# Kernel optimization log

Measured on AMD Instinct MI355X. Metric: run time of the kernel, lower is better.

Reference implementation:

```python
import jax, jax.numpy as jnp
import numpy as np

B, N, H, HEADS = 4, 512, 256, 8
SUBH = H // HEADS
FF = 4 * H
EPS = 1e-5


def _layernorm(x, g, b):
    m = jnp.mean(x, axis=-1, keepdims=True)
    v = jnp.mean(jnp.square(x - m), axis=-1, keepdims=True)
    return (x - m) * jax.lax.rsqrt(v + EPS) * g + b


def setup_inputs() -> dict:
    key = jax.random.key(0)
    ks = jax.random.split(key, 10)
    sc = 0.02
    return {
        "S": jax.random.normal(ks[0], (B, N, H), dtype=jnp.float32),
        "T": jax.random.normal(ks[1], (B, N, N, H), dtype=jnp.float32),
        "masks": jnp.ones((B, N), dtype=bool),
        "Wqk": jax.random.normal(ks[2], (H, HEADS), dtype=jnp.float32) * sc,
        "Wv": jax.random.normal(ks[3], (H, H), dtype=jnp.float32) * sc,
        "bv": jnp.zeros((H,), dtype=jnp.float32),
        "Wo": jax.random.normal(ks[4], (H, H), dtype=jnp.float32) * sc,
        "bo": jnp.zeros((H,), dtype=jnp.float32),
        "g0": jnp.ones((H,), dtype=jnp.float32),
        "beta0": jnp.zeros((H,), dtype=jnp.float32),
        "W1": jax.random.normal(ks[5], (H, FF), dtype=jnp.float32) * sc,
        "b1": jnp.zeros((FF,), dtype=jnp.float32),
        "W2": jax.random.normal(ks[6], (FF, H), dtype=jnp.float32) * sc,
        "b2": jnp.zeros((H,), dtype=jnp.float32),
        "g1": jnp.ones((H,), dtype=jnp.float32),
        "beta1": jnp.zeros((H,), dtype=jnp.float32),
    }


def reference(S, T, masks, Wqk, Wv, bv, Wo, bo, g0, beta0, W1, b1, W2, b2, g1, beta1):
    # pairwise mask: [B,N,N], additive -1000 where masked
    mask2 = masks[:, None, :] & masks[:, :, None]
    add = -1000.0 * (1.0 - mask2.astype(jnp.float32))

    # attention scores: linear projection of pairwise tensor T -> [B, heads, N, N]
    attn = jnp.einsum('bije,eh->bhij', T, Wqk) + add[:, None, :, :]
    attn = jax.nn.softmax(attn, axis=-1)

    # values: [B, heads, N, subH]
    v = (S @ Wv + bv).reshape(B, N, HEADS, SUBH).transpose(0, 2, 1, 3)
    ctx = jnp.einsum('bhij,bhjd->bhid', attn, v)  # [B, heads, N, subH]
    ctx = ctx.transpose(0, 2, 1, 3).reshape(B, N, H)

    x = jax.nn.relu(ctx @ Wo + bo)
    x = _layernorm(S + x, g0, beta0)

    y = jax.nn.relu(x @ W1 + b1) @ W2 + b2
    out = _layernorm(x + y, g1, beta1)
    return (out, attn)
```

## Files before the change

### kernel.cpp

```cpp
#include <hip/hip_runtime.h>
#include <hip/hip_bf16.h>
#include <cstddef>

#define NB 4
#define NN 512
#define NH 256
#define NHEADS 8
#define NSUBH 32
#define NFF 1024
#define LNEPS 1e-5f

using short8 = __attribute__((ext_vector_type(8))) short;
using f32x4  = __attribute__((ext_vector_type(4))) float;
using fvec4  = __attribute__((ext_vector_type(4))) float;

__device__ __forceinline__ unsigned short f2bf(float x) {
    __hip_bfloat16 h = __float2bfloat16(x);
    return *reinterpret_cast<unsigned short*>(&h);
}

__global__ __launch_bounds__(64) void prep_wqk_kernel(
    const float* __restrict__ Wqk, short8* __restrict__ wqk_bf)
{
    const int lane = threadIdx.x;
    const int n = lane & 15;
    #pragma unroll
    for (int ks = 0; ks < 8; ++ks) {
        short8 v;
        #pragma unroll
        for (int q = 0; q < 8; ++q) {
            const int k = ks * 32 + ((lane >> 4) & 3) * 8 + q;
            v[q] = (n < 8) ? (short)f2bf(Wqk[k * NHEADS + n]) : (short)0;
        }
        wqk_bf[ks * 64 + lane] = v;
    }
}

__global__ __launch_bounds__(256) void vproj_kernel(
    const float* __restrict__ S, const float* __restrict__ Wv,
    const float* __restrict__ bv, float* __restrict__ v_ws)
{
    __shared__ float srow[8][NH];
    const int t = threadIdx.x;
    const int row0 = blockIdx.x * 8;
    #pragma unroll
    for (int r = 0; r < 8; ++r) srow[r][t] = S[(size_t)(row0 + r) * NH + t];
    __syncthreads();

    float acc[8];
    #pragma unroll
    for (int r = 0; r < 8; ++r) acc[r] = 0.0f;
    for (int e = 0; e < NH; e += 4) {
        const float w0 = Wv[(size_t)(e + 0) * NH + t];
        const float w1 = Wv[(size_t)(e + 1) * NH + t];
        const float w2 = Wv[(size_t)(e + 2) * NH + t];
        const float w3 = Wv[(size_t)(e + 3) * NH + t];
        #pragma unroll
        for (int r = 0; r < 8; ++r) {
            const float4 x4 = *(const float4*)&srow[r][e];
            acc[r] = fmaf(x4.x, w0, fmaf(x4.y, w1, fmaf(x4.z, w2, fmaf(x4.w, w3, acc[r]))));
        }
    }
    const float bvc = bv[t];
    const int h = t >> 5, d = t & 31;
    const int b = row0 / NN;
    const int jbase = row0 & (NN - 1);
    #pragma unroll
    for (int r = 0; r < 8; ++r)
        v_ws[((size_t)(b * NHEADS + h) * NN + (size_t)(jbase + r)) * NSUBH + d] = acc[r] + bvc;
}

__global__ __launch_bounds__(256, 4) void scores_kernel(
    const float* __restrict__ T, const short8* __restrict__ wqk_bf,
    float* __restrict__ scores)
{
    __shared__ unsigned short tlds[64 * 256];
    const int t = threadIdx.x;
    const int lane = t & 63, wv = t >> 6;
    const int bi = blockIdx.x >> 3;
    const int jt = blockIdx.x & 7;
    const int jbase = jt * 64;

    const fvec4* Tv = (const fvec4*)(T + ((size_t)bi * NN + jbase) * NH);

    fvec4 ga[16];
    #pragma unroll
    for (int i = 0; i < 16; ++i)
        ga[i] = __builtin_nontemporal_load(&Tv[(size_t)(16 * wv + i) * 64 + lane]);

    short8 bfrag[8];
    #pragma unroll
    for (int ks = 0; ks < 8; ++ks) bfrag[ks] = wqk_bf[ks * 64 + lane];

    #pragma unroll
    for (int i = 0; i < 16; ++i) {
        const int row = 16 * wv + i;
        unsigned short v[4];
        v[0] = f2bf(ga[i][0]); v[1] = f2bf(ga[i][1]);
        v[2] = f2bf(ga[i][2]); v[3] = f2bf(ga[i][3]);
        const int byte = (row * 512 + lane * 8) ^ ((row & 7) << 4);
        *(uint2*)((char*)tlds + byte) = *(const uint2*)v;
    }

    f32x4 acc = {0.0f, 0.0f, 0.0f, 0.0f};
    const int jr = 16 * wv + (lane & 15);
    #pragma unroll
    for (int ks = 0; ks < 8; ++ks) {
        const int byte = (jr * 512 + ks * 64 + (lane >> 4) * 16) ^ ((jr & 7) << 4);
        const short8 af = *(const short8*)((const char*)tlds + byte);
        acc = __builtin_amdgcn_mfma_f32_16x16x32_bf16(af, bfrag[ks], acc, 0, 0, 0);
    }

    const int h = lane & 15;
    if (h < 8) {
        const int b = bi >> 9, i = bi & (NN - 1);
        const int j0 = jbase + 16 * wv + (lane >> 4) * 4;
        float4 st;
        st.x = acc[0]; st.y = acc[1]; st.z = acc[2]; st.w = acc[3];
        *(float4*)&scores[((size_t)(b * NHEADS + h) * NN + i) * NN + j0] = st;
    }
}

__global__ __launch_bounds__(256) void softmax_ctx_kernel(
    const int* __restrict__ masks, const float* __restrict__ v_ws,
    float* __restrict__ attn, float* __restrict__ ctx_out)
{
    __shared__ float sc[NN][9];
    __shared__ float maddv[NN];
    const int t = threadIdx.x;
    const int b = blockIdx.x >> 9;
    const int i = blockIdx.x & (NN - 1);

    const int mi = masks[b * NN + i];
    for (int j = t; j < NN; j += 256)
        maddv[j] = (mi != 0 && masks[b * NN + j] != 0) ? 0.0f : -1000.0f;
    __syncthreads();

    const int h = t >> 5;
    const int l32 = t & 31;
    float* srow = attn + ((size_t)(b * NHEADS + h) * NN + i) * NN;

    float vals[16];
    float m = -1e30f;
    #pragma unroll
    for (int k = 0; k < 4; ++k) {
        const int j0 = 4 * l32 + 128 * k;
        float4 s4 = *(const float4*)&srow[j0];
        const float4 m4 = *(const float4*)&maddv[j0];
        s4.x += m4.x; s4.y += m4.y; s4.z += m4.z; s4.w += m4.w;
        vals[4 * k + 0] = s4.x; vals[4 * k + 1] = s4.y;
        vals[4 * k + 2] = s4.z; vals[4 * k + 3] = s4.w;
        m = fmaxf(m, fmaxf(fmaxf(s4.x, s4.y), fmaxf(s4.z, s4.w)));
    }
    #pragma unroll
    for (int off = 16; off >= 1; off >>= 1) m = fmaxf(m, __shfl_xor(m, off, 32));
    float sum = 0.0f;
    #pragma unroll
    for (int k = 0; k < 16; ++k) {
        const float e = __expf(vals[k] - m);
        vals[k] = e;
        sum += e;
    }
    #pragma unroll
    for (int off = 16; off >= 1; off >>= 1) sum += __shfl_xor(sum, off, 32);
    const float inv = 1.0f / sum;
    #pragma unroll
    for (int k = 0; k < 4; ++k) {
        const int j0 = 4 * l32 + 128 * k;
        float4 p4;
        p4.x = vals[4 * k + 0] * inv; p4.y = vals[4 * k + 1] * inv;
        p4.z = vals[4 * k + 2] * inv; p4.w = vals[4 * k + 3] * inv;
        *(float4*)&srow[j0] = p4;
        sc[j0 + 0][h] = p4.x; sc[j0 + 1][h] = p4.y;
        sc[j0 + 2][h] = p4.z; sc[j0 + 3][h] = p4.w;
    }
    __syncthreads();

    const int d = l32;
    const float* vp = v_ws + (size_t)(b * NHEADS + h) * NN * NSUBH + d;
    float acc = 0.0f;
    #pragma unroll 8
    for (int j = 0; j < NN; ++j)
        acc = fmaf(sc[j][h], vp[(size_t)j * NSUBH], acc);
    ctx_out[(size_t)(b * NN + i) * NH + h * NSUBH + d] = acc;
}

__global__ __launch_bounds__(256) void tail_kernel(
    const float* __restrict__ ctx, const float* __restrict__ S,
    const float* __restrict__ Wo, const float* __restrict__ bo,
    const float* __restrict__ g0, const float* __restrict__ beta0,
    const float* __restrict__ W1, const float* __restrict__ b1,
    const float* __restrict__ W2, const float* __restrict__ b2,
    const float* __restrict__ g1, const float* __restrict__ beta1,
    float* __restrict__ out)
{
    __shared__ float xin[8][NH];
    __shared__ float x1[8][NH];
    __shared__ float ybuf[8][NFF];
    const int t = threadIdx.x;
    const int row0 = blockIdx.x * 8;

    #pragma unroll
    for (int r = 0; r < 8; ++r) xin[r][t] = ctx[(size_t)(row0 + r) * NH + t];
    __syncthreads();

    float acc[8];
    #pragma unroll
    for (int r = 0; r < 8; ++r) acc[r] = 0.0f;
    for (int e = 0; e < NH; e += 4) {
        const float w0 = Wo[(size_t)(e + 0) * NH + t];
        const float w1 = Wo[(size_t)(e + 1) * NH + t];
        const float w2 = Wo[(size_t)(e + 2) * NH + t];
        const float w3 = Wo[(size_t)(e + 3) * NH + t];
        #pragma unroll
        for (int r = 0; r < 8; ++r) {
            const float4 x4 = *(const float4*)&xin[r][e];
            acc[r] = fmaf(x4.x, w0, fmaf(x4.y, w1, fmaf(x4.z, w2, fmaf(x4.w, w3, acc[r]))));
        }
    }
    const float boc = bo[t];
    #pragma unroll
    for (int r = 0; r < 8; ++r) {
        const float xv = fmaxf(acc[r] + boc, 0.0f);
        x1[r][t] = S[(size_t)(row0 + r) * NH + t] + xv;
    }
    __syncthreads();

    {
        const int wv = t >> 6, ln = t & 63;
        #pragma unroll
        for (int rr = 0; rr < 2; ++rr) {
            const int r = wv * 2 + rr;
            float s1 = 0.0f, s2 = 0.0f;
            #pragma unroll
            for (int k = 0; k < 4; ++k) {
                const float z = x1[r][ln + 64 * k];
                s1 += z; s2 += z * z;
            }
            #pragma unroll
            for (int off = 32; off >= 1; off >>= 1) {
                s1 += __shfl_xor(s1, off);
                s2 += __shfl_xor(s2, off);
            }
            const float mu = s1 * (1.0f / NH);
            const float rsig = rsqrtf(s2 * (1.0f / NH) - mu * mu + LNEPS);
            #pragma unroll
            for (int k = 0; k < 4; ++k) {
                const int c = ln + 64 * k;
                x1[r][c] = (x1[r][c] - mu) * rsig * g0[c] + beta0[c];
            }
        }
    }
    __syncthreads();

    float acc2[8][4];
    #pragma unroll
    for (int r = 0; r < 8; ++r)
        #pragma unroll
        for (int q = 0; q < 4; ++q) acc2[r][q] = 0.0f;
    for (int e = 0; e < NH; e += 4) {
        float4 x4[8];
        #pragma unroll
        for (int r = 0; r < 8; ++r) x4[r] = *(const float4*)&x1[r][e];
        #pragma unroll
        for (int q = 0; q < 4; ++q) {
            const float* wc = W1 + (size_t)e * NFF + (t + 256 * q);
            const float w0 = wc[0 * NFF], w1 = wc[1 * NFF], w2 = wc[2 * NFF], w3 = wc[3 * NFF];
            #pragma unroll
            for (int r = 0; r < 8; ++r)
                acc2[r][q] = fmaf(x4[r].x, w0, fmaf(x4[r].y, w1, fmaf(x4[r].z, w2, fmaf(x4[r].w, w3, acc2[r][q]))));
        }
    }
    #pragma unroll
    for (int q = 0; q < 4; ++q) {
        const float b1c = b1[t + 256 * q];
        #pragma unroll
        for (int r = 0; r < 8; ++r)
            ybuf[r][t + 256 * q] = fmaxf(acc2[r][q] + b1c, 0.0f);
    }
    __syncthreads();

    float acc3[8];
    #pragma unroll
    for (int r = 0; r < 8; ++r) acc3[r] = 0.0f;
    for (int f = 0; f < NFF; f += 4) {
        const float w0 = W2[(size_t)(f + 0) * NH + t];
        const float w1 = W2[(size_t)(f + 1) * NH + t];
        const float w2 = W2[(size_t)(f + 2) * NH + t];
        const float w3 = W2[(size_t)(f + 3) * NH + t];
        #pragma unroll
        for (int r = 0; r < 8; ++r) {
            const float4 y4 = *(const float4*)&ybuf[r][f];
            acc3[r] = fmaf(y4.x, w0, fmaf(y4.y, w1, fmaf(y4.z, w2, fmaf(y4.w, w3, acc3[r]))));
        }
    }
    const float b2c = b2[t];
    #pragma unroll
    for (int r = 0; r < 8; ++r)
        xin[r][t] = x1[r][t] + acc3[r] + b2c;
    __syncthreads();

    {
        const int wv = t >> 6, ln = t & 63;
        #pragma unroll
        for (int rr = 0; rr < 2; ++rr) {
            const int r = wv * 2 + rr;
            float s1 = 0.0f, s2 = 0.0f;
            #pragma unroll
            for (int k = 0; k < 4; ++k) {
                const float z = xin[r][ln + 64 * k];
                s1 += z; s2 += z * z;
            }
            #pragma unroll
            for (int off = 32; off >= 1; off >>= 1) {
                s1 += __shfl_xor(s1, off);
                s2 += __shfl_xor(s2, off);
            }
            const float mu = s1 * (1.0f / NH);
            const float rsig = rsqrtf(s2 * (1.0f / NH) - mu * mu + LNEPS);
            #pragma unroll
            for (int k = 0; k < 4; ++k) {
                const int c = ln + 64 * k;
                out[(size_t)(row0 + r) * NH + c] = (xin[r][c] - mu) * rsig * g1[c] + beta1[c];
            }
        }
    }
}

extern "C" void kernel_launch(void* const* d_in, const int* in_sizes, int n_in,
                              void* d_out, int out_size, void* d_ws, size_t ws_size,
                              hipStream_t stream) {
    const float* S     = (const float*)d_in[0];
    const float* T     = (const float*)d_in[1];
    const int*   masks = (const int*)  d_in[2];
    const float* Wqk   = (const float*)d_in[3];
    const float* Wv    = (const float*)d_in[4];
    const float* bv    = (const float*)d_in[5];
    const float* Wo    = (const float*)d_in[6];
    const float* bo    = (const float*)d_in[7];
    const float* g0    = (const float*)d_in[8];
    const float* beta0 = (const float*)d_in[9];
    const float* W1    = (const float*)d_in[10];
    const float* b1    = (const float*)d_in[11];
    const float* W2    = (const float*)d_in[12];
    const float* b2    = (const float*)d_in[13];
    const float* g1    = (const float*)d_in[14];
    const float* beta1 = (const float*)d_in[15];

    float* out      = (float*)d_out;
    float* attn_out = out + (size_t)NB * NN * NH;
    float* v_ws     = (float*)d_ws;
    short8* wqk_bf  = (short8*)((char*)d_ws + (size_t)NB * NHEADS * NN * NSUBH * 4);
    float* ctx      = out;

    prep_wqk_kernel<<<1, 64, 0, stream>>>(Wqk, wqk_bf);
    vproj_kernel<<<NB * NN / 8, 256, 0, stream>>>(S, Wv, bv, v_ws);
    scores_kernel<<<NB * NN * 8, 256, 0, stream>>>(T, wqk_bf, attn_out);
    softmax_ctx_kernel<<<NB * NN, 256, 0, stream>>>(masks, v_ws, attn_out, ctx);
    tail_kernel<<<NB * NN / 8, 256, 0, stream>>>(ctx, S, Wo, bo, g0, beta0,
                                                 W1, b1, W2, b2, g1, beta1, out);
}
```

Measured before the change: 339.7 us.

## Fuse score projection with softmax and context into one attention kernel

Merges the T-projection scores kernel and the softmax/context kernel so each block handles one query row (all 512 keys, all heads). Scores stay in shared memory instead of going to global attn and being read back, which removes one full write and read of the B*H*N*N score tensor. In exchange each wave loops over 8 tiles with less parallelism per block, there are fewer blocks, and occupancy is reduced via launch bounds of 3 and larger LDS use.

```diff
diff --git a/kernel.cpp b/kernel.cpp
--- a/kernel.cpp
+++ b/kernel.cpp
@@ -70,82 +70,70 @@
         v_ws[((size_t)(b * NHEADS + h) * NN + (size_t)(jbase + r)) * NSUBH + d] = acc[r] + bvc;
 }
 
-__global__ __launch_bounds__(256, 4) void scores_kernel(
+__global__ __launch_bounds__(256, 3) void attn_fused_kernel(
     const float* __restrict__ T, const short8* __restrict__ wqk_bf,
-    float* __restrict__ scores)
-{
-    __shared__ unsigned short tlds[64 * 256];
-    const int t = threadIdx.x;
-    const int lane = t & 63, wv = t >> 6;
-    const int bi = blockIdx.x >> 3;
-    const int jt = blockIdx.x & 7;
-    const int jbase = jt * 64;
-
-    const fvec4* Tv = (const fvec4*)(T + ((size_t)bi * NN + jbase) * NH);
-
-    fvec4 ga[16];
-    #pragma unroll
-    for (int i = 0; i < 16; ++i)
-        ga[i] = __builtin_nontemporal_load(&Tv[(size_t)(16 * wv + i) * 64 + lane]);
-
-    short8 bfrag[8];
-    #pragma unroll
-    for (int ks = 0; ks < 8; ++ks) bfrag[ks] = wqk_bf[ks * 64 + lane];
-
-    #pragma unroll
-    for (int i = 0; i < 16; ++i) {
-        const int row = 16 * wv + i;
-        unsigned short v[4];
-        v[0] = f2bf(ga[i][0]); v[1] = f2bf(ga[i][1]);
-        v[2] = f2bf(ga[i][2]); v[3] = f2bf(ga[i][3]);
-        const int byte = (row * 512 + lane * 8) ^ ((row & 7) << 4);
-        *(uint2*)((char*)tlds + byte) = *(const uint2*)v;
-    }
-
-    f32x4 acc = {0.0f, 0.0f, 0.0f, 0.0f};
-    const int jr = 16 * wv + (lane & 15);
-    #pragma unroll
-    for (int ks = 0; ks < 8; ++ks) {
-        const int byte = (jr * 512 + ks * 64 + (lane >> 4) * 16) ^ ((jr & 7) << 4);
-        const short8 af = *(const short8*)((const char*)tlds + byte);
-        acc = __builtin_amdgcn_mfma_f32_16x16x32_bf16(af, bfrag[ks], acc, 0, 0, 0);
-    }
-
-    const int h = lane & 15;
-    if (h < 8) {
-        const int b = bi >> 9, i = bi & (NN - 1);
-        const int j0 = jbase + 16 * wv + (lane >> 4) * 4;
-        float4 st;
-        st.x = acc[0]; st.y = acc[1]; st.z = acc[2]; st.w = acc[3];
-        *(float4*)&scores[((size_t)(b * NHEADS + h) * NN + i) * NN + j0] = st;
-    }
-}
-
-__global__ __launch_bounds__(256) void softmax_ctx_kernel(
     const int* __restrict__ masks, const float* __restrict__ v_ws,
     float* __restrict__ attn, float* __restrict__ ctx_out)
 {
-    __shared__ float sc[NN][9];
+    __shared__ unsigned short tlds[4 * 16 * 256];
+    __shared__ float sc2[NHEADS][516];
     __shared__ float maddv[NN];
     const int t = threadIdx.x;
-    const int b = blockIdx.x >> 9;
-    const int i = blockIdx.x & (NN - 1);
+    const int lane = t & 63, wv = t >> 6;
+    const int bi = blockIdx.x;
+    const int b = bi >> 9, i = bi & (NN - 1);
 
     const int mi = masks[b * NN + i];
     for (int j = t; j < NN; j += 256)
         maddv[j] = (mi != 0 && masks[b * NN + j] != 0) ? 0.0f : -1000.0f;
-    __syncthreads();
-
-    const int h = t >> 5;
+
+    short8 bfrag[8];
+    #pragma unroll
+    for (int ks = 0; ks < 8; ++ks) bfrag[ks] = wqk_bf[ks * 64 + lane];
+
+    const fvec4* Tv = (const fvec4*)(T + (size_t)bi * NN * NH);
+    char* slice = (char*)tlds + wv * 8192;
+    const int h = lane & 15;
+    const int jrl = lane & 15;
+
+    for (int tile = 0; tile < 8; ++tile) {
+        const int jb = wv * 128 + tile * 16;
+        fvec4 ga[16];
+        #pragma unroll
+        for (int r = 0; r < 16; ++r)
+            ga[r] = __builtin_nontemporal_load(&Tv[(size_t)(jb + r) * 64 + lane]);
+        #pragma unroll
+        for (int r = 0; r < 16; ++r) {
+            unsigned short v[4];
+            v[0] = f2bf(ga[r][0]); v[1] = f2bf(ga[r][1]);
+            v[2] = f2bf(ga[r][2]); v[3] = f2bf(ga[r][3]);
+            const int byte = (r * 512 + lane * 8) ^ ((r & 7) << 4);
+            *(uint2*)(slice + byte) = *(const uint2*)v;
+        }
+        f32x4 acc = {0.0f, 0.0f, 0.0f, 0.0f};
+        #pragma unroll
+        for (int ks = 0; ks < 8; ++ks) {
+            const int byte = (jrl * 512 + ks * 64 + (lane >> 4) * 16) ^ ((jrl & 7) << 4);
+            const short8 af = *(const short8*)(slice + byte);
+            acc = __builtin_amdgcn_mfma_f32_16x16x32_bf16(af, bfrag[ks], acc, 0, 0, 0);
+        }
+        if (h < 8) {
+            const int j0 = jb + (lane >> 4) * 4;
+            *(float4*)&sc2[h][j0] = make_float4(acc[0], acc[1], acc[2], acc[3]);
+        }
+    }
+    __syncthreads();
+
+    const int sh = t >> 5;
     const int l32 = t & 31;
-    float* srow = attn + ((size_t)(b * NHEADS + h) * NN + i) * NN;
+    float* arow = attn + ((size_t)(b * NHEADS + sh) * NN + i) * NN;
 
     float vals[16];
     float m = -1e30f;
     #pragma unroll
     for (int k = 0; k < 4; ++k) {
         const int j0 = 4 * l32 + 128 * k;
-        float4 s4 = *(const float4*)&srow[j0];
+        float4 s4 = *(const float4*)&sc2[sh][j0];
         const float4 m4 = *(const float4*)&maddv[j0];
         s4.x += m4.x; s4.y += m4.y; s4.z += m4.z; s4.w += m4.w;
         vals[4 * k + 0] = s4.x; vals[4 * k + 1] = s4.y;
@@ -170,19 +158,18 @@
         float4 p4;
         p4.x = vals[4 * k + 0] * inv; p4.y = vals[4 * k + 1] * inv;
         p4.z = vals[4 * k + 2] * inv; p4.w = vals[4 * k + 3] * inv;
-        *(float4*)&srow[j0] = p4;
-        sc[j0 + 0][h] = p4.x; sc[j0 + 1][h] = p4.y;
-        sc[j0 + 2][h] = p4.z; sc[j0 + 3][h] = p4.w;
+        *(float4*)&arow[j0] = p4;
+        *(float4*)&sc2[sh][j0] = p4;
     }
     __syncthreads();
 
     const int d = l32;
-    const float* vp = v_ws + (size_t)(b * NHEADS + h) * NN * NSUBH + d;
+    const float* vp = v_ws + (size_t)(b * NHEADS + sh) * NN * NSUBH + d;
     float acc = 0.0f;
     #pragma unroll 8
     for (int j = 0; j < NN; ++j)
-        acc = fmaf(sc[j][h], vp[(size_t)j * NSUBH], acc);
-    ctx_out[(size_t)(b * NN + i) * NH + h * NSUBH + d] = acc;
+        acc = fmaf(sc2[sh][j], vp[(size_t)j * NSUBH], acc);
+    ctx_out[(size_t)(b * NN + i) * NH + sh * NSUBH + d] = acc;
 }
 
 __global__ __launch_bounds__(256) void tail_kernel(
@@ -355,8 +342,8 @@
 
     prep_wqk_kernel<<<1, 64, 0, stream>>>(Wqk, wqk_bf);
     vproj_kernel<<<NB * NN / 8, 256, 0, stream>>>(S, Wv, bv, v_ws);
-    scores_kernel<<<NB * NN * 8, 256, 0, stream>>>(T, wqk_bf, attn_out);
-    softmax_ctx_kernel<<<NB * NN, 256, 0, stream>>>(masks, v_ws, attn_out, ctx);
+    attn_fused_kernel<<<NB * NN, 256, 0, stream>>>(T, wqk_bf, masks, v_ws,
+                                                   attn_out, ctx);
     tail_kernel<<<NB * NN / 8, 256, 0, stream>>>(ctx, S, Wo, bo, g0, beta0,
                                                  W1, b1, W2, b2, g1, beta1, out);
 }
```

Measured after the change: 326.8 us. 3.8% less time.
